# Kernel tuning notes

Measured on AMD Instinct MI355X. Metric: run time of the kernel, lower is better.

## Reference

```python
import jax, jax.numpy as jnp
import numpy as np

N_NODES = 50000
N_EDGES = 800000
D = 128  # d_feat == hidden_channels


def setup_inputs() -> dict:
    key = jax.random.key(0)
    ks = jax.random.split(key, 7)
    s = 1.0 / np.sqrt(D)
    return {
        "x": jax.random.normal(ks[0], (N_NODES, D), dtype=jnp.float32),
        "edge_index": jax.random.randint(ks[1], (2, N_EDGES), 0, N_NODES, dtype=jnp.int64),
        "W1_l": jax.random.normal(ks[2], (D, D), dtype=jnp.float32) * s,
        "b1": jnp.zeros((D,), dtype=jnp.float32),
        "W1_r": jax.random.normal(ks[3], (D, D), dtype=jnp.float32) * s,
        "W2_l": jax.random.normal(ks[4], (D, D), dtype=jnp.float32) * s,
        "b2": jnp.zeros((D,), dtype=jnp.float32),
        "W2_r": jax.random.normal(ks[5], (D, D), dtype=jnp.float32) * s,
    }


def reference(x, edge_index, W1_l, b1, W1_r, W2_l, b2, W2_r):
    src = edge_index[0]
    dst = edge_index[1]
    n = x.shape[0]
    # in-degree for mean aggregation (zero-degree nodes get 0 aggregate)
    deg = jax.ops.segment_sum(jnp.ones_like(src, dtype=x.dtype), dst, num_segments=n)
    inv_deg = (1.0 / jnp.maximum(deg, 1.0))[:, None]  # [N,1]

    def sage_conv(h, Wl, b, Wr):
        # mean over incoming neighbor messages, then lin_l(agg) + lin_r(h)
        agg = jax.ops.segment_sum(h[src], dst, num_segments=n) * inv_deg  # [N,D]
        return agg @ Wl + b + h @ Wr

    h = jax.nn.relu(sage_conv(x, W1_l, b1, W1_r))
    return sage_conv(h, W2_l, b2, W2_r)
```

## Files before the change

### kernel.cpp

```cpp
#include <hip/hip_runtime.h>
#include <hip/hip_bf16.h>

typedef __attribute__((ext_vector_type(8))) short bf16x8;
typedef __attribute__((ext_vector_type(4))) float f32x4;

#define CAP 64
#define SH  8

static __device__ inline unsigned short f2b(float f) {
    unsigned u = __float_as_uint(f);
    unsigned r = (u + 0x7FFFu + ((u >> 16) & 1u)) >> 16;
    return (unsigned short)r;
}
static __device__ inline float blo(unsigned u) { return __uint_as_float(u << 16); }
static __device__ inline float bhi(unsigned u) { return __uint_as_float(u & 0xFFFF0000u); }
static __device__ inline unsigned pk_fp8x4(float a, float b, float c, float d) {
    int v = __builtin_amdgcn_cvt_pk_fp8_f32(a, b, 0, false);
    v = __builtin_amdgcn_cvt_pk_fp8_f32(c, d, v, true);
    return (unsigned)v;
}

__global__ void zero_kernel(int* __restrict__ p, int n) {
    int i = blockIdx.x * blockDim.x + threadIdx.x;
    if (i < n) p[i] = 0;
}

__global__ __launch_bounds__(256) void fill_shard_kernel(
        const int* __restrict__ ei, int* __restrict__ cursor,
        unsigned short* __restrict__ edge16, int E, int N, int G, int npg) {
    int s = blockIdx.x & (SH - 1);
    int i = blockIdx.x >> 3;
    int d_lo = s * npg;
    int d_hi = d_lo + npg; if (d_hi > N) d_hi = N;
    int C = (E + G - 1) / G;
    int e0 = i * C;
    int e1 = e0 + C; if (e1 > E) e1 = E;
    for (int e = e0 + threadIdx.x; e < e1; e += 256) {
        int d = ei[E + e];
        if (d < d_lo || d >= d_hi) continue;
        int src = ei[e];
        if ((unsigned)src >= (unsigned)N) src = 0;
        int pos = atomicAdd(&cursor[d], 1);
        if (pos < CAP) edge16[(size_t)d * CAP + pos] = (unsigned short)src;
    }
}

__global__ __launch_bounds__(256) void convert_kernel(
        const float* __restrict__ x, unsigned short* __restrict__ xb,
        unsigned char* __restrict__ xf8, int n4,
        const float* __restrict__ W1l, const float* __restrict__ W1r,
        const float* __restrict__ W2l, const float* __restrict__ W2r,
        unsigned short* __restrict__ wt, int G1) {
    int b = blockIdx.x;
    if (b < G1) {
        int i = b * 256 + threadIdx.x;
        if (i >= n4) return;
        float4 v = ((const float4*)x)[i];
        ushort4 o;
        o.x = f2b(v.x); o.y = f2b(v.y); o.z = f2b(v.z); o.w = f2b(v.w);
        ((ushort4*)xb)[i] = o;
        ((unsigned*)xf8)[i] = pk_fp8x4(v.x, v.y, v.z, v.w);
    } else {
        int id = (b - G1) * 256 + threadIdx.x;
        int layer = id >> 15;
        int rem = id & 32767;
        int n = rem >> 8;
        int kk = rem & 255;
        const float* Wlp = layer ? W2l : W1l;
        const float* Wrp = layer ? W2r : W1r;
        float v = (kk < 128) ? Wlp[(size_t)kk * 128 + n]
                             : Wrp[(size_t)(kk - 128) * 128 + n];
        wt[(size_t)layer * 32768 + (size_t)n * 256 + kk] = f2b(v);
    }
}

__global__ __launch_bounds__(256) void b2f8_kernel(
        const unsigned short* __restrict__ hb, unsigned char* __restrict__ h8, int n8) {
    int i = blockIdx.x * blockDim.x + threadIdx.x;
    if (i >= n8) return;
    uint4 v = ((const uint4*)hb)[i];
    uint2 o;
    o.x = pk_fp8x4(blo(v.x), bhi(v.x), blo(v.y), bhi(v.y));
    o.y = pk_fp8x4(blo(v.z), bhi(v.z), blo(v.w), bhi(v.w));
    ((uint2*)h8)[i] = o;
}

__global__ __launch_bounds__(256) void aggregate_f8_kernel(
        const unsigned char* __restrict__ in8, const int* __restrict__ cursor,
        const unsigned short* __restrict__ edge16, const int* __restrict__ ei,
        unsigned short* __restrict__ agg, int E, int N) {
    int node = blockIdx.x * 4 + (threadIdx.x >> 6);
    if (node >= N) return;
    int lane = threadIdx.x & 63;
    int g = lane >> 3;
    int f = lane & 7;
    int deg = cursor[node];

    float acc[16];
    #pragma unroll
    for (int t = 0; t < 16; ++t) acc[t] = 0.f;

    if (deg <= CAP) {
        const unsigned short* base = edge16 + (size_t)node * CAP;
        int idx = (lane < deg) ? (int)base[lane] : 0;
        #pragma unroll 2
        for (int j = 0; j < deg; j += 8) {
            int e = j + g;
            int s = __shfl(idx, e & 63);
            if (e < deg) {
                uint4 v = *(const uint4*)(in8 + (size_t)s * 128 + f * 16);
                #pragma unroll
                for (int w = 0; w < 4; ++w) {
                    unsigned dw = (&v.x)[w];
                    acc[w * 4 + 0] += __builtin_amdgcn_cvt_f32_fp8(dw, 0);
                    acc[w * 4 + 1] += __builtin_amdgcn_cvt_f32_fp8(dw, 1);
                    acc[w * 4 + 2] += __builtin_amdgcn_cvt_f32_fp8(dw, 2);
                    acc[w * 4 + 3] += __builtin_amdgcn_cvt_f32_fp8(dw, 3);
                }
            }
        }
    } else {
        for (int j = 0; j < E; j += 8) {
            int e = j + g;
            bool act = (e < E) && (ei[E + e] == node);
            if (act) {
                int s = ei[e];
                if ((unsigned)s >= (unsigned)N) s = 0;
                uint4 v = *(const uint4*)(in8 + (size_t)s * 128 + f * 16);
                #pragma unroll
                for (int w = 0; w < 4; ++w) {
                    unsigned dw = (&v.x)[w];
                    acc[w * 4 + 0] += __builtin_amdgcn_cvt_f32_fp8(dw, 0);
                    acc[w * 4 + 1] += __builtin_amdgcn_cvt_f32_fp8(dw, 1);
                    acc[w * 4 + 2] += __builtin_amdgcn_cvt_f32_fp8(dw, 2);
                    acc[w * 4 + 3] += __builtin_amdgcn_cvt_f32_fp8(dw, 3);
                }
            }
        }
    }

    #pragma unroll
    for (int d = 8; d <= 32; d <<= 1) {
        #pragma unroll
        for (int t = 0; t < 16; ++t) acc[t] += __shfl_xor(acc[t], d);
    }

    if (g == 0) {
        float inv = 1.0f / (float)(deg > 1 ? deg : 1);
        uint4 o0, o1;
        o0.x = (unsigned)f2b(acc[0] * inv)  | ((unsigned)f2b(acc[1] * inv)  << 16);
        o0.y = (unsigned)f2b(acc[2] * inv)  | ((unsigned)f2b(acc[3] * inv)  << 16);
        o0.z = (unsigned)f2b(acc[4] * inv)  | ((unsigned)f2b(acc[5] * inv)  << 16);
        o0.w = (unsigned)f2b(acc[6] * inv)  | ((unsigned)f2b(acc[7] * inv)  << 16);
        o1.x = (unsigned)f2b(acc[8] * inv)  | ((unsigned)f2b(acc[9] * inv)  << 16);
        o1.y = (unsigned)f2b(acc[10] * inv) | ((unsigned)f2b(acc[11] * inv) << 16);
        o1.z = (unsigned)f2b(acc[12] * inv) | ((unsigned)f2b(acc[13] * inv) << 16);
        o1.w = (unsigned)f2b(acc[14] * inv) | ((unsigned)f2b(acc[15] * inv) << 16);
        unsigned short* dst = agg + (size_t)node * 128 + f * 16;
        *(uint4*)dst = o0;
        *(uint4*)(dst + 8) = o1;
    }
}

template<int RELU, int OUT_BF16>
__global__ __launch_bounds__(256) void gemm_mfma_kernel(
        const unsigned short* __restrict__ Arow, const unsigned short* __restrict__ Xrow,
        const unsigned short* __restrict__ Wt, const float* __restrict__ bias,
        void* __restrict__ outp, int n) {
    constexpr int LDK = 264;
    __shared__ unsigned short sA[64 * LDK];
    int tid = threadIdx.x;
    int row0 = blockIdx.x * 64;

    #pragma unroll
    for (int it = 0; it < 8; ++it) {
        int c = tid + it * 256;
        int r = c >> 5;
        int q = c & 31;
        int row = row0 + r; if (row >= n) row = n - 1;
        uint4 v = (q < 16) ? ((const uint4*)(Arow + (size_t)row * 128))[q]
                           : ((const uint4*)(Xrow + (size_t)row * 128))[q - 16];
        *(uint4*)&sA[r * LDK + q * 8] = v;
    }
    __syncthreads();

    int lane = tid & 63;
    int wave = tid >> 6;
    int quad = lane >> 4;
    int tm   = lane & 15;

    f32x4 acc[4][2];
    #pragma unroll
    for (int m = 0; m < 4; ++m)
        #pragma unroll
        for (int j = 0; j < 2; ++j)
            acc[m][j] = (f32x4){0.f, 0.f, 0.f, 0.f};

    const unsigned short* wb0 = Wt + (size_t)(wave * 32 + tm) * 256;

    #pragma unroll
    for (int ks = 0; ks < 8; ++ks) {
        int k0 = ks * 32 + quad * 8;
        bf16x8 a[4], b[2];
        #pragma unroll
        for (int m = 0; m < 4; ++m)
            a[m] = *(const bf16x8*)&sA[(m * 16 + tm) * LDK + k0];
        #pragma unroll
        for (int j = 0; j < 2; ++j)
            b[j] = *(const bf16x8*)(wb0 + (size_t)j * 16 * 256 + k0);
        #pragma unroll
        for (int m = 0; m < 4; ++m)
            #pragma unroll
            for (int j = 0; j < 2; ++j)
                acc[m][j] = __builtin_amdgcn_mfma_f32_16x16x32_bf16(a[m], b[j], acc[m][j], 0, 0, 0);
    }

    #pragma unroll
    for (int j = 0; j < 2; ++j) {
        int ncol = wave * 32 + j * 16 + tm;
        float bb = bias[ncol];
        #pragma unroll
        for (int m = 0; m < 4; ++m) {
            #pragma unroll
            for (int reg = 0; reg < 4; ++reg) {
                int row = row0 + m * 16 + quad * 4 + reg;
                if (row >= n) continue;
                float v = acc[m][j][reg] + bb;
                if (RELU) v = v > 0.f ? v : 0.f;
                if (OUT_BF16)
                    ((unsigned short*)outp)[(size_t)row * 128 + ncol] = f2b(v);
                else
                    ((float*)outp)[(size_t)row * 128 + ncol] = v;
            }
        }
    }
}

extern "C" void kernel_launch(void* const* d_in, const int* in_sizes, int n_in,
                              void* d_out, int out_size, void* d_ws, size_t ws_size,
                              hipStream_t stream) {
    const float* x   = (const float*)d_in[0];
    const int*   ei  = (const int*)d_in[1];
    const float* W1l = (const float*)d_in[2];
    const float* b1  = (const float*)d_in[3];
    const float* W1r = (const float*)d_in[4];
    const float* W2l = (const float*)d_in[5];
    const float* b2  = (const float*)d_in[6];
    const float* W2r = (const float*)d_in[7];
    float* out = (float*)d_out;

    const int D = 128;
    const int N = in_sizes[0] / D;
    const int E = in_sizes[1] / 2;

    char* ws = (char*)d_ws;
    size_t off = 0;
    auto alloc = [&](size_t bytes) {
        size_t o = off;
        off = (off + bytes + 511) & ~(size_t)511;
        return (void*)(ws + o);
    };
    int*            cursor  = (int*)           alloc((size_t)N * 4);
    unsigned short* edge16  = (unsigned short*)alloc((size_t)N * CAP * 2);
    unsigned short* agg_bf  = (unsigned short*)alloc((size_t)N * D * 2);
    unsigned short* xb      = (unsigned short*)alloc((size_t)N * D * 2);
    unsigned char*  xf8     = (unsigned char*) alloc((size_t)N * D);
    unsigned short* wt      = (unsigned short*)alloc((size_t)2 * 128 * 256 * 2);
    unsigned short* h_bf = xb;
    unsigned char*  h_f8 = xf8;
    (void)ws_size; (void)n_in; (void)out_size;

    zero_kernel<<<(N + 255) / 256, 256, 0, stream>>>(cursor, N);
    {
        int G = 256;
        int npg = (N + SH - 1) / SH;
        fill_shard_kernel<<<SH * G, 256, 0, stream>>>(ei, cursor, edge16, E, N, G, npg);
    }

    int n4 = N * D / 4;
    int G1 = (n4 + 255) / 256;
    convert_kernel<<<G1 + 256, 256, 0, stream>>>(x, xb, xf8, n4, W1l, W1r, W2l, W2r, wt, G1);
    const unsigned short* wt1 = wt;
    const unsigned short* wt2 = wt + (size_t)128 * 256;

    int agg_grid  = (N + 3) / 4;
    int gemm_grid = (N + 63) / 64;
    int n8 = N * D / 8;

    aggregate_f8_kernel<<<agg_grid, 256, 0, stream>>>(xf8, cursor, edge16, ei, agg_bf, E, N);
    gemm_mfma_kernel<1, 1><<<gemm_grid, 256, 0, stream>>>(agg_bf, xb, wt1, b1, (void*)h_bf, N);

    b2f8_kernel<<<(n8 + 255) / 256, 256, 0, stream>>>(h_bf, h_f8, n8);
    aggregate_f8_kernel<<<agg_grid, 256, 0, stream>>>(h_f8, cursor, edge16, ei, agg_bf, E, N);
    gemm_mfma_kernel<0, 0><<<gemm_grid, 256, 0, stream>>>(agg_bf, h_bf, wt2, b2, (void*)out, N);
}
```

Measured before the change: 234.9 us.

## Fuse the whole two-layer SAGE pipeline into one cooperative persistent kernel

Replaces the seven separate launches (zero, fill, convert, two aggregates, two GEMMs, bf16-to-fp8 conversion) with a single cooperative persistent kernel. Its phases are separated by grid-wide syncs and use grid-stride loops over nodes and tiles. The layer-1 GEMM epilogue now writes the fp8 copy of h directly, which removes the separate b2f8 pass. The goal is to cut launch overhead, inter-kernel gaps and one full read/write of h. The costs are grid-sync overhead, a grid capped by occupancy (at most 1024 blocks) that limits how many gathers are in flight, and byte-granular fp8 stores. A multi-kernel fallback path is kept in case the cooperative launch fails.

```diff
diff --git a/kernel.cpp b/kernel.cpp
--- a/kernel.cpp
+++ b/kernel.cpp
@@ -1,11 +1,14 @@
 #include <hip/hip_runtime.h>
 #include <hip/hip_bf16.h>
+#include <hip/hip_cooperative_groups.h>
+
+namespace cg = cooperative_groups;
 
 typedef __attribute__((ext_vector_type(8))) short bf16x8;
 typedef __attribute__((ext_vector_type(4))) float f32x4;
 
 #define CAP 64
-#define SH  8
+#define LDK 264
 
 static __device__ inline unsigned short f2b(float f) {
     unsigned u = __float_as_uint(f);
@@ -19,49 +22,28 @@
     v = __builtin_amdgcn_cvt_pk_fp8_f32(c, d, v, true);
     return (unsigned)v;
 }
-
-__global__ void zero_kernel(int* __restrict__ p, int n) {
-    int i = blockIdx.x * blockDim.x + threadIdx.x;
-    if (i < n) p[i] = 0;
-}
-
-__global__ __launch_bounds__(256) void fill_shard_kernel(
-        const int* __restrict__ ei, int* __restrict__ cursor,
-        unsigned short* __restrict__ edge16, int E, int N, int G, int npg) {
-    int s = blockIdx.x & (SH - 1);
-    int i = blockIdx.x >> 3;
-    int d_lo = s * npg;
-    int d_hi = d_lo + npg; if (d_hi > N) d_hi = N;
-    int C = (E + G - 1) / G;
-    int e0 = i * C;
-    int e1 = e0 + C; if (e1 > E) e1 = E;
-    for (int e = e0 + threadIdx.x; e < e1; e += 256) {
-        int d = ei[E + e];
-        if (d < d_lo || d >= d_hi) continue;
-        int src = ei[e];
-        if ((unsigned)src >= (unsigned)N) src = 0;
-        int pos = atomicAdd(&cursor[d], 1);
-        if (pos < CAP) edge16[(size_t)d * CAP + pos] = (unsigned short)src;
-    }
-}
-
-__global__ __launch_bounds__(256) void convert_kernel(
-        const float* __restrict__ x, unsigned short* __restrict__ xb,
-        unsigned char* __restrict__ xf8, int n4,
-        const float* __restrict__ W1l, const float* __restrict__ W1r,
-        const float* __restrict__ W2l, const float* __restrict__ W2r,
-        unsigned short* __restrict__ wt, int G1) {
-    int b = blockIdx.x;
-    if (b < G1) {
-        int i = b * 256 + threadIdx.x;
-        if (i >= n4) return;
+static __device__ inline unsigned char f2f8(float v) {
+    return (unsigned char)(__builtin_amdgcn_cvt_pk_fp8_f32(v, v, 0, false) & 0xFF);
+}
+
+
+static __device__ void prep_phase(const float* __restrict__ x,
+                                  unsigned short* __restrict__ xb,
+                                  unsigned char* __restrict__ xf8,
+                                  int* __restrict__ cursor,
+                                  const float* __restrict__ W1l, const float* __restrict__ W1r,
+                                  const float* __restrict__ W2l, const float* __restrict__ W2r,
+                                  unsigned short* __restrict__ wt, int N, int T, int t0) {
+    for (int i = t0; i < N; i += T) cursor[i] = 0;
+    int n4 = N * 32;
+    for (int i = t0; i < n4; i += T) {
         float4 v = ((const float4*)x)[i];
         ushort4 o;
         o.x = f2b(v.x); o.y = f2b(v.y); o.z = f2b(v.z); o.w = f2b(v.w);
         ((ushort4*)xb)[i] = o;
         ((unsigned*)xf8)[i] = pk_fp8x4(v.x, v.y, v.z, v.w);
-    } else {
-        int id = (b - G1) * 256 + threadIdx.x;
+    }
+    for (int id = t0; id < 65536; id += T) {
         int layer = id >> 15;
         int rem = id & 32767;
         int n = rem >> 8;
@@ -74,166 +56,251 @@
     }
 }
 
-__global__ __launch_bounds__(256) void b2f8_kernel(
-        const unsigned short* __restrict__ hb, unsigned char* __restrict__ h8, int n8) {
-    int i = blockIdx.x * blockDim.x + threadIdx.x;
-    if (i >= n8) return;
-    uint4 v = ((const uint4*)hb)[i];
-    uint2 o;
-    o.x = pk_fp8x4(blo(v.x), bhi(v.x), blo(v.y), bhi(v.y));
-    o.y = pk_fp8x4(blo(v.z), bhi(v.z), blo(v.w), bhi(v.w));
-    ((uint2*)h8)[i] = o;
-}
-
-__global__ __launch_bounds__(256) void aggregate_f8_kernel(
+static __device__ void fill_phase(const int* __restrict__ ei, int* __restrict__ cursor,
+                                  unsigned short* __restrict__ edge16, int E, int N,
+                                  int bid, int nblocks) {
+    int s  = bid & 7;
+    int ci = bid >> 3;
+    int G  = nblocks >> 3;
+    int npg = (N + 7) >> 3;
+    int d_lo = s * npg;
+    int d_hi = d_lo + npg; if (d_hi > N) d_hi = N;
+    int C = (E + G - 1) / G;
+    int e0 = ci * C;
+    int e1 = e0 + C; if (e1 > E) e1 = E;
+    for (int e = e0 + (int)threadIdx.x; e < e1; e += 256) {
+        int d = ei[E + e];
+        if (d < d_lo || d >= d_hi) continue;
+        int src = ei[e];
+        if ((unsigned)src >= (unsigned)N) src = 0;
+        int pos = atomicAdd(&cursor[d], 1);
+        if (pos < CAP) edge16[(size_t)d * CAP + pos] = (unsigned short)src;
+    }
+}
+
+static __device__ void agg_phase(const unsigned char* __restrict__ in8,
+                                 const int* __restrict__ cursor,
+                                 const unsigned short* __restrict__ edge16,
+                                 const int* __restrict__ ei,
+                                 unsigned short* __restrict__ agg, int E, int N,
+                                 int bid, int nblocks) {
+    int wave = threadIdx.x >> 6;
+    int lane = threadIdx.x & 63;
+    int g = lane >> 3;
+    int f = lane & 7;
+    for (int base = bid * 4; base < N; base += nblocks * 4) {
+        int node = base + wave;
+        if (node >= N) continue;
+        int deg = cursor[node];
+
+        float acc[16];
+        #pragma unroll
+        for (int t = 0; t < 16; ++t) acc[t] = 0.f;
+
+        if (deg <= CAP) {
+            const unsigned short* basep = edge16 + (size_t)node * CAP;
+            int idx = (lane < deg) ? (int)basep[lane] : 0;
+            #pragma unroll 2
+            for (int j = 0; j < deg; j += 8) {
+                int e = j + g;
+                int s = __shfl(idx, e & 63);
+                if (e < deg) {
+                    uint4 v = *(const uint4*)(in8 + (size_t)s * 128 + f * 16);
+                    #pragma unroll
+                    for (int w = 0; w < 4; ++w) {
+                        unsigned dw = (&v.x)[w];
+                        acc[w * 4 + 0] += __builtin_amdgcn_cvt_f32_fp8(dw, 0);
+                        acc[w * 4 + 1] += __builtin_amdgcn_cvt_f32_fp8(dw, 1);
+                        acc[w * 4 + 2] += __builtin_amdgcn_cvt_f32_fp8(dw, 2);
+                        acc[w * 4 + 3] += __builtin_amdgcn_cvt_f32_fp8(dw, 3);
+                    }
+                }
+            }
+        } else {
+            for (int j = 0; j < E; j += 8) {
+                int e = j + g;
+                bool act = (e < E) && (ei[E + e] == node);
+                if (act) {
+                    int s = ei[e];
+                    if ((unsigned)s >= (unsigned)N) s = 0;
+                    uint4 v = *(const uint4*)(in8 + (size_t)s * 128 + f * 16);
+                    #pragma unroll
+                    for (int w = 0; w < 4; ++w) {
+                        unsigned dw = (&v.x)[w];
+                        acc[w * 4 + 0] += __builtin_amdgcn_cvt_f32_fp8(dw, 0);
+                        acc[w * 4 + 1] += __builtin_amdgcn_cvt_f32_fp8(dw, 1);
+                        acc[w * 4 + 2] += __builtin_amdgcn_cvt_f32_fp8(dw, 2);
+                        acc[w * 4 + 3] += __builtin_amdgcn_cvt_f32_fp8(dw, 3);
+                    }
+                }
+            }
+        }
+
+        #pragma unroll
+        for (int d = 8; d <= 32; d <<= 1) {
+            #pragma unroll
+            for (int t = 0; t < 16; ++t) acc[t] += __shfl_xor(acc[t], d);
+        }
+
+        if (g == 0) {
+            float inv = 1.0f / (float)(deg > 1 ? deg : 1);
+            uint4 o0, o1;
+            o0.x = (unsigned)f2b(acc[0] * inv)  | ((unsigned)f2b(acc[1] * inv)  << 16);
+            o0.y = (unsigned)f2b(acc[2] * inv)  | ((unsigned)f2b(acc[3] * inv)  << 16);
+            o0.z = (unsigned)f2b(acc[4] * inv)  | ((unsigned)f2b(acc[5] * inv)  << 16);
+            o0.w = (unsigned)f2b(acc[6] * inv)  | ((unsigned)f2b(acc[7] * inv)  << 16);
+            o1.x = (unsigned)f2b(acc[8] * inv)  | ((unsigned)f2b(acc[9] * inv)  << 16);
+            o1.y = (unsigned)f2b(acc[10] * inv) | ((unsigned)f2b(acc[11] * inv) << 16);
+            o1.z = (unsigned)f2b(acc[12] * inv) | ((unsigned)f2b(acc[13] * inv) << 16);
+            o1.w = (unsigned)f2b(acc[14] * inv) | ((unsigned)f2b(acc[15] * inv) << 16);
+            unsigned short* dst = agg + (size_t)node * 128 + f * 16;
+            *(uint4*)dst = o0;
+            *(uint4*)(dst + 8) = o1;
+        }
+    }
+}
+
+template<int RELU, int OUT_BF16, int WF8>
+static __device__ void gemm_phase(const unsigned short* __restrict__ Arow,
+                                  const unsigned short* __restrict__ Xrow,
+                                  const unsigned short* __restrict__ Wt,
+                                  const float* __restrict__ bias,
+                                  void* __restrict__ outp,
+                                  unsigned char* __restrict__ f8out, int N,
+                                  unsigned short* sA, int bid, int nblocks) {
+    int tid = threadIdx.x;
+    int ntiles = (N + 63) >> 6;
+    for (int t = bid; t < ntiles; t += nblocks) {
+        int row0 = t * 64;
+        #pragma unroll
+        for (int it = 0; it < 8; ++it) {
+            int c = tid + it * 256;
+            int r = c >> 5;
+            int q = c & 31;
+            int row = row0 + r; if (row >= N) row = N - 1;
+            uint4 v = (q < 16) ? ((const uint4*)(Arow + (size_t)row * 128))[q]
+                               : ((const uint4*)(Xrow + (size_t)row * 128))[q - 16];
+            *(uint4*)&sA[r * LDK + q * 8] = v;
+        }
+        __syncthreads();
+
+        int lane = tid & 63;
+        int wave = tid >> 6;
+        int quad = lane >> 4;
+        int tm   = lane & 15;
+
+        f32x4 acc[4][2];
+        #pragma unroll
+        for (int m = 0; m < 4; ++m)
+            #pragma unroll
+            for (int j = 0; j < 2; ++j)
+                acc[m][j] = (f32x4){0.f, 0.f, 0.f, 0.f};
+
+        const unsigned short* wb0 = Wt + (size_t)(wave * 32 + tm) * 256;
+
+        #pragma unroll
+        for (int ks = 0; ks < 8; ++ks) {
+            int k0 = ks * 32 + quad * 8;
+            bf16x8 a[4], b[2];
+            #pragma unroll
+            for (int m = 0; m < 4; ++m)
+                a[m] = *(const bf16x8*)&sA[(m * 16 + tm) * LDK + k0];
+            #pragma unroll
+            for (int j = 0; j < 2; ++j)
+                b[j] = *(const bf16x8*)(wb0 + (size_t)j * 16 * 256 + k0);
+            #pragma unroll
+            for (int m = 0; m < 4; ++m)
+                #pragma unroll
+                for (int j = 0; j < 2; ++j)
+                    acc[m][j] = __builtin_amdgcn_mfma_f32_16x16x32_bf16(a[m], b[j], acc[m][j], 0, 0, 0);
+        }
+
+        #pragma unroll
+        for (int j = 0; j < 2; ++j) {
+            int ncol = wave * 32 + j * 16 + tm;
+            float bb = bias[ncol];
+            #pragma unroll
+            for (int m = 0; m < 4; ++m) {
+                #pragma unroll
+                for (int reg = 0; reg < 4; ++reg) {
+                    int row = row0 + m * 16 + quad * 4 + reg;
+                    if (row >= N) continue;
+                    float v = acc[m][j][reg] + bb;
+                    if (RELU) v = v > 0.f ? v : 0.f;
+                    if (OUT_BF16)
+                        ((unsigned short*)outp)[(size_t)row * 128 + ncol] = f2b(v);
+                    else
+                        ((float*)outp)[(size_t)row * 128 + ncol] = v;
+                    if (WF8)
+                        f8out[(size_t)row * 128 + ncol] = f2f8(v);
+                }
+            }
+        }
+        __syncthreads();
+    }
+}
+
+extern "C" __global__ void __launch_bounds__(256, 4) mega_kernel(
+        const float* __restrict__ x, const int* __restrict__ ei,
+        const float* __restrict__ W1l, const float* __restrict__ b1,
+        const float* __restrict__ W1r, const float* __restrict__ W2l,
+        const float* __restrict__ b2, const float* __restrict__ W2r,
+        float* __restrict__ out, int* __restrict__ cursor,
+        unsigned short* __restrict__ edge16, unsigned short* __restrict__ agg_bf,
+        unsigned short* __restrict__ xb, unsigned char* __restrict__ xf8,
+        unsigned short* __restrict__ wt, int N, int E) {
+    __shared__ unsigned short sA[64 * LDK];
+    cg::grid_group grid = cg::this_grid();
+    int nb = gridDim.x;
+    int bid = blockIdx.x;
+    int T = nb * 256;
+    int t0 = bid * 256 + threadIdx.x;
+
+    prep_phase(x, xb, xf8, cursor, W1l, W1r, W2l, W2r, wt, N, T, t0);
+    grid.sync();
+    fill_phase(ei, cursor, edge16, E, N, bid, nb);
+    grid.sync();
+    agg_phase(xf8, cursor, edge16, ei, agg_bf, E, N, bid, nb);
+    grid.sync();
+    gemm_phase<1, 1, 1>(agg_bf, xb, wt, b1, (void*)xb, xf8, N, sA, bid, nb);
+    grid.sync();
+    agg_phase(xf8, cursor, edge16, ei, agg_bf, E, N, bid, nb);
+    grid.sync();
+    gemm_phase<0, 0, 0>(agg_bf, xb, wt + 32768, b2, (void*)out, nullptr, N, sA, bid, nb);
+}
+
+__global__ __launch_bounds__(256) void k_prep(
+        const float* __restrict__ x, unsigned short* __restrict__ xb,
+        unsigned char* __restrict__ xf8, int* __restrict__ cursor,
+        const float* __restrict__ W1l, const float* __restrict__ W1r,
+        const float* __restrict__ W2l, const float* __restrict__ W2r,
+        unsigned short* __restrict__ wt, int N) {
+    int T = gridDim.x * 256;
+    int t0 = blockIdx.x * 256 + threadIdx.x;
+    prep_phase(x, xb, xf8, cursor, W1l, W1r, W2l, W2r, wt, N, T, t0);
+}
+
+__global__ __launch_bounds__(256) void k_fill(
+        const int* __restrict__ ei, int* __restrict__ cursor,
+        unsigned short* __restrict__ edge16, int E, int N) {
+    fill_phase(ei, cursor, edge16, E, N, blockIdx.x, gridDim.x);
+}
+
+__global__ __launch_bounds__(256) void k_agg(
         const unsigned char* __restrict__ in8, const int* __restrict__ cursor,
         const unsigned short* __restrict__ edge16, const int* __restrict__ ei,
         unsigned short* __restrict__ agg, int E, int N) {
-    int node = blockIdx.x * 4 + (threadIdx.x >> 6);
-    if (node >= N) return;
-    int lane = threadIdx.x & 63;
-    int g = lane >> 3;
-    int f = lane & 7;
-    int deg = cursor[node];
-
-    float acc[16];
-    #pragma unroll
-    for (int t = 0; t < 16; ++t) acc[t] = 0.f;
-
-    if (deg <= CAP) {
-        const unsigned short* base = edge16 + (size_t)node * CAP;
-        int idx = (lane < deg) ? (int)base[lane] : 0;
-        #pragma unroll 2
-        for (int j = 0; j < deg; j += 8) {
-            int e = j + g;
-            int s = __shfl(idx, e & 63);
-            if (e < deg) {
-                uint4 v = *(const uint4*)(in8 + (size_t)s * 128 + f * 16);
-                #pragma unroll
-                for (int w = 0; w < 4; ++w) {
-                    unsigned dw = (&v.x)[w];
-                    acc[w * 4 + 0] += __builtin_amdgcn_cvt_f32_fp8(dw, 0);
-                    acc[w * 4 + 1] += __builtin_amdgcn_cvt_f32_fp8(dw, 1);
-                    acc[w * 4 + 2] += __builtin_amdgcn_cvt_f32_fp8(dw, 2);
-                    acc[w * 4 + 3] += __builtin_amdgcn_cvt_f32_fp8(dw, 3);
-                }
-            }
-        }
-    } else {
-        for (int j = 0; j < E; j += 8) {
-            int e = j + g;
-            bool act = (e < E) && (ei[E + e] == node);
-            if (act) {
-                int s = ei[e];
-                if ((unsigned)s >= (unsigned)N) s = 0;
-                uint4 v = *(const uint4*)(in8 + (size_t)s * 128 + f * 16);
-                #pragma unroll
-                for (int w = 0; w < 4; ++w) {
-                    unsigned dw = (&v.x)[w];
-                    acc[w * 4 + 0] += __builtin_amdgcn_cvt_f32_fp8(dw, 0);
-                    acc[w * 4 + 1] += __builtin_amdgcn_cvt_f32_fp8(dw, 1);
-                    acc[w * 4 + 2] += __builtin_amdgcn_cvt_f32_fp8(dw, 2);
-                    acc[w * 4 + 3] += __builtin_amdgcn_cvt_f32_fp8(dw, 3);
-                }
-            }
-        }
-    }
-
-    #pragma unroll
-    for (int d = 8; d <= 32; d <<= 1) {
-        #pragma unroll
-        for (int t = 0; t < 16; ++t) acc[t] += __shfl_xor(acc[t], d);
-    }
-
-    if (g == 0) {
-        float inv = 1.0f / (float)(deg > 1 ? deg : 1);
-        uint4 o0, o1;
-        o0.x = (unsigned)f2b(acc[0] * inv)  | ((unsigned)f2b(acc[1] * inv)  << 16);
-        o0.y = (unsigned)f2b(acc[2] * inv)  | ((unsigned)f2b(acc[3] * inv)  << 16);
-        o0.z = (unsigned)f2b(acc[4] * inv)  | ((unsigned)f2b(acc[5] * inv)  << 16);
-        o0.w = (unsigned)f2b(acc[6] * inv)  | ((unsigned)f2b(acc[7] * inv)  << 16);
-        o1.x = (unsigned)f2b(acc[8] * inv)  | ((unsigned)f2b(acc[9] * inv)  << 16);
-        o1.y = (unsigned)f2b(acc[10] * inv) | ((unsigned)f2b(acc[11] * inv) << 16);
-        o1.z = (unsigned)f2b(acc[12] * inv) | ((unsigned)f2b(acc[13] * inv) << 16);
-        o1.w = (unsigned)f2b(acc[14] * inv) | ((unsigned)f2b(acc[15] * inv) << 16);
-        unsigned short* dst = agg + (size_t)node * 128 + f * 16;
-        *(uint4*)dst = o0;
-        *(uint4*)(dst + 8) = o1;
-    }
-}
-
-template<int RELU, int OUT_BF16>
-__global__ __launch_bounds__(256) void gemm_mfma_kernel(
+    agg_phase(in8, cursor, edge16, ei, agg, E, N, blockIdx.x, gridDim.x);
+}
+
+template<int RELU, int OUT_BF16, int WF8>
+__global__ __launch_bounds__(256) void k_gemm(
         const unsigned short* __restrict__ Arow, const unsigned short* __restrict__ Xrow,
         const unsigned short* __restrict__ Wt, const float* __restrict__ bias,
-        void* __restrict__ outp, int n) {
-    constexpr int LDK = 264;
+        void* __restrict__ outp, unsigned char* __restrict__ f8out, int N) {
     __shared__ unsigned short sA[64 * LDK];
-    int tid = threadIdx.x;
-    int row0 = blockIdx.x * 64;
-
-    #pragma unroll
-    for (int it = 0; it < 8; ++it) {
-        int c = tid + it * 256;
-        int r = c >> 5;
-        int q = c & 31;
-        int row = row0 + r; if (row >= n) row = n - 1;
-        uint4 v = (q < 16) ? ((const uint4*)(Arow + (size_t)row * 128))[q]
-                           : ((const uint4*)(Xrow + (size_t)row * 128))[q - 16];
-        *(uint4*)&sA[r * LDK + q * 8] = v;
-    }
-    __syncthreads();
-
-    int lane = tid & 63;
-    int wave = tid >> 6;
-    int quad = lane >> 4;
-    int tm   = lane & 15;
-
-    f32x4 acc[4][2];
-    #pragma unroll
-    for (int m = 0; m < 4; ++m)
-        #pragma unroll
-        for (int j = 0; j < 2; ++j)
-            acc[m][j] = (f32x4){0.f, 0.f, 0.f, 0.f};
-
-    const unsigned short* wb0 = Wt + (size_t)(wave * 32 + tm) * 256;
-
-    #pragma unroll
-    for (int ks = 0; ks < 8; ++ks) {
-        int k0 = ks * 32 + quad * 8;
-        bf16x8 a[4], b[2];
-        #pragma unroll
-        for (int m = 0; m < 4; ++m)
-            a[m] = *(const bf16x8*)&sA[(m * 16 + tm) * LDK + k0];
-        #pragma unroll
-        for (int j = 0; j < 2; ++j)
-            b[j] = *(const bf16x8*)(wb0 + (size_t)j * 16 * 256 + k0);
-        #pragma unroll
-        for (int m = 0; m < 4; ++m)
-            #pragma unroll
-            for (int j = 0; j < 2; ++j)
-                acc[m][j] = __builtin_amdgcn_mfma_f32_16x16x32_bf16(a[m], b[j], acc[m][j], 0, 0, 0);
-    }
-
-    #pragma unroll
-    for (int j = 0; j < 2; ++j) {
-        int ncol = wave * 32 + j * 16 + tm;
-        float bb = bias[ncol];
-        #pragma unroll
-        for (int m = 0; m < 4; ++m) {
-            #pragma unroll
-            for (int reg = 0; reg < 4; ++reg) {
-                int row = row0 + m * 16 + quad * 4 + reg;
-                if (row >= n) continue;
-                float v = acc[m][j][reg] + bb;
-                if (RELU) v = v > 0.f ? v : 0.f;
-                if (OUT_BF16)
-                    ((unsigned short*)outp)[(size_t)row * 128 + ncol] = f2b(v);
-                else
-                    ((float*)outp)[(size_t)row * 128 + ncol] = v;
-            }
-        }
-    }
+    gemm_phase<RELU, OUT_BF16, WF8>(Arow, Xrow, Wt, bias, outp, f8out, N, sA,
+                                    blockIdx.x, gridDim.x);
 }
 
 extern "C" void kernel_launch(void* const* d_in, const int* in_sizes, int n_in,
@@ -250,8 +317,8 @@
     float* out = (float*)d_out;
 
     const int D = 128;
-    const int N = in_sizes[0] / D;
-    const int E = in_sizes[1] / 2;
+    int N = in_sizes[0] / D;
+    int E = in_sizes[1] / 2;
 
     char* ws = (char*)d_ws;
     size_t off = 0;
@@ -266,31 +333,39 @@
     unsigned short* xb      = (unsigned short*)alloc((size_t)N * D * 2);
     unsigned char*  xf8     = (unsigned char*) alloc((size_t)N * D);
     unsigned short* wt      = (unsigned short*)alloc((size_t)2 * 128 * 256 * 2);
-    unsigned short* h_bf = xb;
-    unsigned char*  h_f8 = xf8;
     (void)ws_size; (void)n_in; (void)out_size;
 
-    zero_kernel<<<(N + 255) / 256, 256, 0, stream>>>(cursor, N);
-    {
-        int G = 256;
-        int npg = (N + SH - 1) / SH;
-        fill_shard_kernel<<<SH * G, 256, 0, stream>>>(ei, cursor, edge16, E, N, G, npg);
-    }
-
-    int n4 = N * D / 4;
-    int G1 = (n4 + 255) / 256;
-    convert_kernel<<<G1 + 256, 256, 0, stream>>>(x, xb, xf8, n4, W1l, W1r, W2l, W2r, wt, G1);
-    const unsigned short* wt1 = wt;
-    const unsigned short* wt2 = wt + (size_t)128 * 256;
-
-    int agg_grid  = (N + 3) / 4;
-    int gemm_grid = (N + 63) / 64;
-    int n8 = N * D / 8;
-
-    aggregate_f8_kernel<<<agg_grid, 256, 0, stream>>>(xf8, cursor, edge16, ei, agg_bf, E, N);
-    gemm_mfma_kernel<1, 1><<<gemm_grid, 256, 0, stream>>>(agg_bf, xb, wt1, b1, (void*)h_bf, N);
-
-    b2f8_kernel<<<(n8 + 255) / 256, 256, 0, stream>>>(h_bf, h_f8, n8);
-    aggregate_f8_kernel<<<agg_grid, 256, 0, stream>>>(h_f8, cursor, edge16, ei, agg_bf, E, N);
-    gemm_mfma_kernel<0, 0><<<gemm_grid, 256, 0, stream>>>(agg_bf, h_bf, wt2, b2, (void*)out, N);
-}
+    int dev = 0;
+    hipGetDevice(&dev);
+    int nCU = 256;
+    hipDeviceGetAttribute(&nCU, hipDeviceAttributeMultiprocessorCount, dev);
+    int perCU = 0;
+    hipError_t qerr = hipOccupancyMaxActiveBlocksPerMultiprocessor(
+        &perCU, (const void*)mega_kernel, 256, 0);
+    long cap = (qerr == hipSuccess) ? (long)perCU * nCU : 0;
+    int grid = (int)(cap < 1024 ? cap : 1024);
+    grid &= ~7;
+
+    hipError_t err = hipErrorUnknown;
+    if (grid >= 8) {
+        void* args[] = {
+            (void*)&x, (void*)&ei, (void*)&W1l, (void*)&b1, (void*)&W1r,
+            (void*)&W2l, (void*)&b2, (void*)&W2r, (void*)&out,
+            (void*)&cursor, (void*)&edge16, (void*)&agg_bf, (void*)&xb,
+            (void*)&xf8, (void*)&wt, (void*)&N, (void*)&E
+        };
+        err = hipLaunchCooperativeKernel((void*)mega_kernel, dim3(grid), dim3(256),
+                                         args, 0, stream);
+    }
+
+    if (err != hipSuccess) {
+        k_prep<<<1024, 256, 0, stream>>>(x, xb, xf8, cursor, W1l, W1r, W2l, W2r, wt, N);
+        k_fill<<<2048, 256, 0, stream>>>(ei, cursor, edge16, E, N);
+        int agg_grid = (N + 3) / 4;
+        int gemm_grid = (N + 63) / 64;
+        k_agg<<<agg_grid, 256, 0, stream>>>(xf8, cursor, edge16, ei, agg_bf, E, N);
+        k_gemm<1, 1, 1><<<gemm_grid, 256, 0, stream>>>(agg_bf, xb, wt, b1, (void*)xb, xf8, N);
+        k_agg<<<agg_grid, 256, 0, stream>>>(xf8, cursor, edge16, ei, agg_bf, E, N);
+        k_gemm<0, 0, 0><<<gemm_grid, 256, 0, stream>>>(agg_bf, xb, wt + 32768, b2, (void*)out, nullptr, N);
+    }
+}
```

Result: slower. 245.6 us (+4.6%).
